# Performance work log

Hardware: AMD Instinct MI355X
Metric: run time of the kernel (lower is better)

The kernel has to match this reference:

```python
import jax, jax.numpy as jnp
import numpy as np

N_AQI, N_MEO = 35, 18
F_OUT = 16
ALPHA = 0.2


def _xavier(k, shape, gain=1.414):
    fan_in, fan_out = shape
    limit = gain * (6.0 / (fan_in + fan_out)) ** 0.5
    return jax.random.uniform(k, shape, jnp.float32, -limit, limit)


def setup_inputs() -> dict:
    key = jax.random.key(0)
    ks = jax.random.split(key, 16)
    B, T = 32, 32
    N = N_AQI + N_MEO
    out_aqi = jax.random.normal(ks[0], (B, T, N_AQI, 1), jnp.float32)
    out_meo = jax.random.normal(ks[1], (B, T, N_MEO, 3), jnp.float32)
    # sparse-ish adjacency with self loops; adj_norm is a (masked) float weight
    adj = (jax.random.uniform(ks[2], (N, N)) < 0.3).astype(jnp.float32)
    adj = adj.at[jnp.arange(N), jnp.arange(N)].set(1.0)
    adj_norm = adj * jax.random.uniform(ks[3], (N, N), jnp.float32)
    inp = {
        "out_aqi": out_aqi,
        "out_meo": out_meo,
        "adj": adj,
        "adj_norm": adj_norm,
        "W_trans": _xavier(ks[4], (1, 6), gain=1.0),
        "b_trans": jnp.zeros((6,), jnp.float32),
        "W_xa": _xavier(ks[5], (6, F_OUT)),
        "W_xm": _xavier(ks[6], (3, F_OUT)),
        "W_ua": _xavier(ks[7], (6, F_OUT)),
        "W_um": _xavier(ks[8], (3, F_OUT)),
        "a_aa": _xavier(ks[9], (2 * F_OUT + 1, 1)),
        "a_am": _xavier(ks[10], (2 * F_OUT + 1, 1)),
        "a_ma": _xavier(ks[11], (2 * F_OUT + 1, 1)),
        "a_mm": _xavier(ks[12], (2 * F_OUT + 1, 1)),
        "W_out": _xavier(ks[13], (32, 1), gain=1.0),
        "b_out": jnp.zeros((1,), jnp.float32),
    }
    return inp


def _lrelu(x):
    return jnp.where(x > 0, x, ALPHA * x)


def _edge_block(h_src, h_dst, anorm_blk, a):
    # Equivalent to matmul(cat[h_i, h_j, adj_norm_ij], a) without materializing
    # the dense (BT, Ni, Nj, 2F+1) tensor: split a into src/dst/adj parts.
    s = h_src @ a[:F_OUT, 0]                 # (BT, Ni)
    d = h_dst @ a[F_OUT:2 * F_OUT, 0]        # (BT, Nj)
    return _lrelu(s[:, :, None] + d[:, None, :] + anorm_blk[None, :, :] * a[2 * F_OUT, 0])


def reference(out_aqi, out_meo, adj, adj_norm, W_trans, b_trans, W_xa, W_xm,
              W_ua, W_um, a_aa, a_am, a_ma, a_mm, W_out, b_out):
    B, T = out_aqi.shape[:2]
    BT = B * T
    aqi = out_aqi.reshape(BT, N_AQI, 1) @ W_trans + b_trans    # (BT, 35, 6)
    meo = out_meo.reshape(BT, N_MEO, 3)                         # (BT, 18, 3)

    heter_attri = jnp.concatenate([aqi @ W_xa, meo @ W_xm], axis=1)  # (BT, 53, 16)
    h_aqi = aqi @ W_ua                                          # (BT, 35, 16)
    h_meo = meo @ W_um                                          # (BT, 18, 16)

    an = adj_norm
    e_aa = _edge_block(h_aqi, h_aqi, an[:N_AQI, :N_AQI], a_aa)
    e_am = _edge_block(h_aqi, h_meo, an[:N_AQI, N_AQI:], a_am)
    e_ma = _edge_block(h_meo, h_aqi, an[N_AQI:, :N_AQI], a_ma)
    e_mm = _edge_block(h_meo, h_meo, an[N_AQI:, N_AQI:], a_mm)
    e = jnp.concatenate([
        jnp.concatenate([e_aa, e_am], axis=2),
        jnp.concatenate([e_ma, e_mm], axis=2),
    ], axis=1)                                                  # (BT, 53, 53)

    att = jnp.where(adj[None, :, :] > 0, e, -1e12)
    att = jax.nn.softmax(att, axis=2)
    heter_out = att @ heter_attri                               # (BT, 53, 16)

    m_aqi = jnp.mean(heter_out[:, :N_AQI, :], axis=1)
    m_meo = jnp.mean(heter_out[:, N_AQI:, :], axis=1)
    out_smetric = jax.nn.sigmoid(jnp.concatenate([m_aqi, m_meo], axis=1))  # (BT, 32)
    out_sscore = jax.nn.sigmoid(out_smetric @ W_out + b_out)               # (BT, 1)
    return out_sscore, out_smetric
```

## Files before the change

kernel.cpp:

```cpp
#include <hip/hip_runtime.h>

#define N_AQI 35
#define N_MEO 18
#define NN    53
#define F     16
#define AP    20

__global__ __launch_bounds__(256)
void spat_disc_kernel(
    const float* __restrict__ out_aqi,
    const float* __restrict__ out_meo,
    const float* __restrict__ adj,
    const float* __restrict__ adj_norm,
    const float* __restrict__ W_trans,
    const float* __restrict__ b_trans,
    const float* __restrict__ W_xa,
    const float* __restrict__ W_xm,
    const float* __restrict__ W_ua,
    const float* __restrict__ W_um,
    const float* __restrict__ a_aa,
    const float* __restrict__ a_am,
    const float* __restrict__ a_ma,
    const float* __restrict__ a_mm,
    const float* __restrict__ W_out,
    const float* __restrict__ b_out,
    float* __restrict__ out, int BT)
{
  const int bt  = blockIdx.x;
  const int tid = threadIdx.x;
  const int i   = tid >> 2;
  const int fq  = tid & 3;

  __shared__ float sh_wxa[F], sh_bxa[F], sh_wua[F], sh_bua[F];
  __shared__ float sh_c[8];
  __shared__ float sh_v[12];
  __shared__ float sh_l[4];
  __shared__ float sh_dA[NN];
  __shared__ float sh_dM[NN];
  __shared__ float sh_attri[NN * AP];
  __shared__ float sh_P[NN * NN];
  __shared__ float sh_ho[NN * AP];
  __shared__ float sh_sm[32];

  if (tid < F) {
    float wxa = 0.f, bxa = 0.f, wua = 0.f, bua = 0.f;
    for (int k = 0; k < 6; ++k) {
      float wt = W_trans[k], btr = b_trans[k];
      wxa += wt  * W_xa[k * F + tid];
      bxa += btr * W_xa[k * F + tid];
      wua += wt  * W_ua[k * F + tid];
      bua += btr * W_ua[k * F + tid];
    }
    sh_wxa[tid] = wxa; sh_bxa[tid] = bxa;
    sh_wua[tid] = wua; sh_bua[tid] = bua;
  }
  __syncthreads();

  if (tid < 8) {
    const float* avec = (tid == 0 || tid == 1 || tid == 4 || tid == 5) ? a_aa
                       : (tid < 4 ? a_am : a_ma);
    int off = (tid < 4) ? 0 : F;
    const float* wv = (tid & 1) ? sh_bua : sh_wua;
    float acc = 0.f;
    for (int f = 0; f < F; ++f) acc += wv[f] * avec[off + f];
    sh_c[tid] = acc;
  } else if (tid < 20) {
    int t = tid - 8;
    int k = t % 3;
    int grp = t / 3;
    const float* avec = (grp == 0) ? a_ma : (grp == 1) ? a_mm
                       : (grp == 2) ? a_am : a_mm;
    int off = (grp < 2) ? 0 : F;
    float acc = 0.f;
    for (int f = 0; f < F; ++f) acc += W_um[k * F + f] * avec[off + f];
    sh_v[t] = acc;
  } else if (tid < 24) {
    const float* avec = (tid == 20) ? a_aa : (tid == 21) ? a_am
                       : (tid == 22) ? a_ma : a_mm;
    sh_l[tid - 20] = avec[2 * F];
  }
  __syncthreads();

  if (tid < NN) {
    if (tid < N_AQI) {
      float x = out_aqi[bt * N_AQI + tid];
      sh_dA[tid] = sh_c[4] * x + sh_c[5];
      sh_dM[tid] = sh_c[6] * x + sh_c[7];
      for (int f = 0; f < F; ++f)
        sh_attri[tid * AP + f] = sh_wxa[f] * x + sh_bxa[f];
    } else {
      int m = tid - N_AQI;
      float m0 = out_meo[(bt * N_MEO + m) * 3 + 0];
      float m1 = out_meo[(bt * N_MEO + m) * 3 + 1];
      float m2 = out_meo[(bt * N_MEO + m) * 3 + 2];
      sh_dA[tid] = m0 * sh_v[6] + m1 * sh_v[7]  + m2 * sh_v[8];
      sh_dM[tid] = m0 * sh_v[9] + m1 * sh_v[10] + m2 * sh_v[11];
      for (int f = 0; f < F; ++f)
        sh_attri[tid * AP + f] = m0 * W_xm[0 * F + f] + m1 * W_xm[1 * F + f] + m2 * W_xm[2 * F + f];
    }
  }
  for (int t = tid; t < NN * NN; t += 256) {
    int ii = t / NN;
    int jj = t - ii * NN;
    float a  = adj[t];
    float an = adj_norm[t];
    float l  = (ii < N_AQI) ? ((jj < N_AQI) ? sh_l[0] : sh_l[1])
                            : ((jj < N_AQI) ? sh_l[2] : sh_l[3]);
    sh_P[t] = (a > 0.f) ? an * l : -INFINITY;
  }
  float s0 = 0.f, s1 = 0.f;
  if (i < NN) {
    if (i < N_AQI) {
      float x = out_aqi[bt * N_AQI + i];
      s0 = sh_c[0] * x + sh_c[1];
      s1 = sh_c[2] * x + sh_c[3];
    } else {
      int m = i - N_AQI;
      float m0 = out_meo[(bt * N_MEO + m) * 3 + 0];
      float m1 = out_meo[(bt * N_MEO + m) * 3 + 1];
      float m2 = out_meo[(bt * N_MEO + m) * 3 + 2];
      s0 = m0 * sh_v[0] + m1 * sh_v[1] + m2 * sh_v[2];
      s1 = m0 * sh_v[3] + m1 * sh_v[4] + m2 * sh_v[5];
    }
  }
  __syncthreads();

  if (i < NN) {
    const float* dbase = (i < N_AQI) ? sh_dA : sh_dM;
    const float* Prow  = sh_P + i * NN;
    float a0 = 0.f, a1 = 0.f, a2 = 0.f, a3 = 0.f, lsum = 0.f;
#pragma unroll 1
    for (int j = 0; j < NN; ++j) {
      float z = ((j < N_AQI) ? s0 : s1) + dbase[j] + Prow[j];
      float e = (z > 0.0f) ? z : 0.2f * z;
      float w = __expf(e);
      lsum += w;
      const float4 av = *(const float4*)(sh_attri + j * AP + fq * 4);
      a0 += w * av.x; a1 += w * av.y; a2 += w * av.z; a3 += w * av.w;
    }
    float inv = 1.0f / lsum;
    float4* hrow = (float4*)(sh_ho + i * AP + fq * 4);
    *hrow = make_float4(a0 * inv, a1 * inv, a2 * inv, a3 * inv);
  }
  __syncthreads();

  if (tid < 32) {
    float s = 0.f;
    if (tid < F) {
      for (int r = 0; r < N_AQI; ++r) s += sh_ho[r * AP + tid];
      s *= (1.0f / N_AQI);
    } else {
      int f = tid - F;
      for (int r = N_AQI; r < NN; ++r) s += sh_ho[r * AP + f];
      s *= (1.0f / N_MEO);
    }
    float sm = 1.0f / (1.0f + __expf(-s));
    sh_sm[tid] = sm;
    out[BT + bt * 32 + tid] = sm;
  }
  __syncthreads();

  if (tid == 0) {
    float z = b_out[0];
    for (int k = 0; k < 32; ++k) z += sh_sm[k] * W_out[k];
    out[bt] = 1.0f / (1.0f + __expf(-z));
  }
}

extern "C" void kernel_launch(void* const* d_in, const int* in_sizes, int n_in,
                              void* d_out, int out_size, void* d_ws, size_t ws_size,
                              hipStream_t stream) {
  const float* out_aqi  = (const float*)d_in[0];
  const float* out_meo  = (const float*)d_in[1];
  const float* adj      = (const float*)d_in[2];
  const float* adj_norm = (const float*)d_in[3];
  const float* W_trans  = (const float*)d_in[4];
  const float* b_trans  = (const float*)d_in[5];
  const float* W_xa     = (const float*)d_in[6];
  const float* W_xm     = (const float*)d_in[7];
  const float* W_ua     = (const float*)d_in[8];
  const float* W_um     = (const float*)d_in[9];
  const float* a_aa     = (const float*)d_in[10];
  const float* a_am     = (const float*)d_in[11];
  const float* a_ma     = (const float*)d_in[12];
  const float* a_mm     = (const float*)d_in[13];
  const float* W_out    = (const float*)d_in[14];
  const float* b_out    = (const float*)d_in[15];
  float* out = (float*)d_out;

  const int BT = in_sizes[0] / N_AQI;

  spat_disc_kernel<<<BT, 256, 0, stream>>>(
      out_aqi, out_meo, adj, adj_norm, W_trans, b_trans,
      W_xa, W_xm, W_ua, W_um, a_aa, a_am, a_ma, a_mm, W_out, b_out,
      out, BT);
}
```

Baseline: 99.18 us.

## Hoist batch-invariant weight folding and masked adjacency into a precompute kernel

Adds a small precompute kernel that folds the weight products and builds the masked, scaled adjacency matrix once into workspace, instead of every one of the 1024 blocks redoing it. The main kernel now reads the P matrix straight from global memory (likely L2-cached) instead of shared memory, unrolls the inner attention loop by 4, and replaces the final serial 32-element dot product with a warp shuffle reduction. The trade-offs are an extra kernel launch and global-memory reads in the hot loop where shared-memory reads were used before, but shared memory use and per-block setup syncs go down.

```diff
diff --git a/kernel.cpp b/kernel.cpp
--- a/kernel.cpp
+++ b/kernel.cpp
@@ -5,25 +5,74 @@
 #define NN    53
 #define F     16
 #define AP    20
+#define P_OFF 64
+
+__global__ __launch_bounds__(256)
+void precompute_kernel(
+    const float* __restrict__ adj, const float* __restrict__ adj_norm,
+    const float* __restrict__ W_trans, const float* __restrict__ b_trans,
+    const float* __restrict__ W_xa, const float* __restrict__ W_ua,
+    const float* __restrict__ W_um,
+    const float* __restrict__ a_aa, const float* __restrict__ a_am,
+    const float* __restrict__ a_ma, const float* __restrict__ a_mm,
+    float* __restrict__ wsf)
+{
+  const int tid = threadIdx.x;
+  __shared__ float s_wua[F], s_bua[F];
+
+  if (blockIdx.x == 0) {
+    if (tid < F) {
+      float wxa = 0.f, bxa = 0.f, wua = 0.f, bua = 0.f;
+      for (int k = 0; k < 6; ++k) {
+        float wt = W_trans[k], btr = b_trans[k];
+        wxa += wt  * W_xa[k * F + tid];
+        bxa += btr * W_xa[k * F + tid];
+        wua += wt  * W_ua[k * F + tid];
+        bua += btr * W_ua[k * F + tid];
+      }
+      s_wua[tid] = wua; s_bua[tid] = bua;
+      wsf[20 + tid] = wxa; wsf[36 + tid] = bxa;
+    }
+    __syncthreads();
+    if (tid < 8) {
+      const float* avec = (tid == 0 || tid == 1 || tid == 4 || tid == 5) ? a_aa
+                         : (tid < 4 ? a_am : a_ma);
+      int off = (tid < 4) ? 0 : F;
+      const float* wv = (tid & 1) ? s_bua : s_wua;
+      float acc = 0.f;
+      for (int f = 0; f < F; ++f) acc += wv[f] * avec[off + f];
+      wsf[tid] = acc;
+    } else if (tid < 20) {
+      int t = tid - 8;
+      int k = t % 3;
+      int grp = t / 3;
+      const float* avec = (grp == 0) ? a_ma : (grp == 1) ? a_mm
+                         : (grp == 2) ? a_am : a_mm;
+      int off = (grp < 2) ? 0 : F;
+      float acc = 0.f;
+      for (int f = 0; f < F; ++f) acc += W_um[k * F + f] * avec[off + f];
+      wsf[8 + t] = acc;
+    }
+  }
+
+  const float l0 = a_aa[2 * F], l1 = a_am[2 * F], l2 = a_ma[2 * F], l3 = a_mm[2 * F];
+  for (int t = blockIdx.x * 256 + tid; t < NN * NN; t += 8 * 256) {
+    int ii = t / NN;
+    int jj = t - ii * NN;
+    float l = (ii < N_AQI) ? ((jj < N_AQI) ? l0 : l1)
+                           : ((jj < N_AQI) ? l2 : l3);
+    wsf[P_OFF + t] = (adj[t] > 0.f) ? adj_norm[t] * l : -INFINITY;
+  }
+}
 
 __global__ __launch_bounds__(256)
 void spat_disc_kernel(
     const float* __restrict__ out_aqi,
     const float* __restrict__ out_meo,
-    const float* __restrict__ adj,
-    const float* __restrict__ adj_norm,
-    const float* __restrict__ W_trans,
-    const float* __restrict__ b_trans,
-    const float* __restrict__ W_xa,
     const float* __restrict__ W_xm,
-    const float* __restrict__ W_ua,
-    const float* __restrict__ W_um,
-    const float* __restrict__ a_aa,
-    const float* __restrict__ a_am,
-    const float* __restrict__ a_ma,
-    const float* __restrict__ a_mm,
     const float* __restrict__ W_out,
     const float* __restrict__ b_out,
+    const float* __restrict__ wsf,
     float* __restrict__ out, int BT)
 {
   const int bt  = blockIdx.x;
@@ -31,105 +80,55 @@
   const int i   = tid >> 2;
   const int fq  = tid & 3;
 
-  __shared__ float sh_wxa[F], sh_bxa[F], sh_wua[F], sh_bua[F];
-  __shared__ float sh_c[8];
-  __shared__ float sh_v[12];
-  __shared__ float sh_l[4];
+  __shared__ float shc[52];
   __shared__ float sh_dA[NN];
   __shared__ float sh_dM[NN];
   __shared__ float sh_attri[NN * AP];
-  __shared__ float sh_P[NN * NN];
   __shared__ float sh_ho[NN * AP];
-  __shared__ float sh_sm[32];
 
-  if (tid < F) {
-    float wxa = 0.f, bxa = 0.f, wua = 0.f, bua = 0.f;
-    for (int k = 0; k < 6; ++k) {
-      float wt = W_trans[k], btr = b_trans[k];
-      wxa += wt  * W_xa[k * F + tid];
-      bxa += btr * W_xa[k * F + tid];
-      wua += wt  * W_ua[k * F + tid];
-      bua += btr * W_ua[k * F + tid];
-    }
-    sh_wxa[tid] = wxa; sh_bxa[tid] = bxa;
-    sh_wua[tid] = wua; sh_bua[tid] = bua;
-  }
-  __syncthreads();
-
-  if (tid < 8) {
-    const float* avec = (tid == 0 || tid == 1 || tid == 4 || tid == 5) ? a_aa
-                       : (tid < 4 ? a_am : a_ma);
-    int off = (tid < 4) ? 0 : F;
-    const float* wv = (tid & 1) ? sh_bua : sh_wua;
-    float acc = 0.f;
-    for (int f = 0; f < F; ++f) acc += wv[f] * avec[off + f];
-    sh_c[tid] = acc;
-  } else if (tid < 20) {
-    int t = tid - 8;
-    int k = t % 3;
-    int grp = t / 3;
-    const float* avec = (grp == 0) ? a_ma : (grp == 1) ? a_mm
-                       : (grp == 2) ? a_am : a_mm;
-    int off = (grp < 2) ? 0 : F;
-    float acc = 0.f;
-    for (int f = 0; f < F; ++f) acc += W_um[k * F + f] * avec[off + f];
-    sh_v[t] = acc;
-  } else if (tid < 24) {
-    const float* avec = (tid == 20) ? a_aa : (tid == 21) ? a_am
-                       : (tid == 22) ? a_ma : a_mm;
-    sh_l[tid - 20] = avec[2 * F];
-  }
+  if (tid < 52) shc[tid] = wsf[tid];
   __syncthreads();
 
   if (tid < NN) {
     if (tid < N_AQI) {
       float x = out_aqi[bt * N_AQI + tid];
-      sh_dA[tid] = sh_c[4] * x + sh_c[5];
-      sh_dM[tid] = sh_c[6] * x + sh_c[7];
+      sh_dA[tid] = shc[4] * x + shc[5];
+      sh_dM[tid] = shc[6] * x + shc[7];
       for (int f = 0; f < F; ++f)
-        sh_attri[tid * AP + f] = sh_wxa[f] * x + sh_bxa[f];
+        sh_attri[tid * AP + f] = shc[20 + f] * x + shc[36 + f];
     } else {
       int m = tid - N_AQI;
       float m0 = out_meo[(bt * N_MEO + m) * 3 + 0];
       float m1 = out_meo[(bt * N_MEO + m) * 3 + 1];
       float m2 = out_meo[(bt * N_MEO + m) * 3 + 2];
-      sh_dA[tid] = m0 * sh_v[6] + m1 * sh_v[7]  + m2 * sh_v[8];
-      sh_dM[tid] = m0 * sh_v[9] + m1 * sh_v[10] + m2 * sh_v[11];
+      sh_dA[tid] = m0 * shc[8 + 6] + m1 * shc[8 + 7]  + m2 * shc[8 + 8];
+      sh_dM[tid] = m0 * shc[8 + 9] + m1 * shc[8 + 10] + m2 * shc[8 + 11];
       for (int f = 0; f < F; ++f)
         sh_attri[tid * AP + f] = m0 * W_xm[0 * F + f] + m1 * W_xm[1 * F + f] + m2 * W_xm[2 * F + f];
     }
-  }
-  for (int t = tid; t < NN * NN; t += 256) {
-    int ii = t / NN;
-    int jj = t - ii * NN;
-    float a  = adj[t];
-    float an = adj_norm[t];
-    float l  = (ii < N_AQI) ? ((jj < N_AQI) ? sh_l[0] : sh_l[1])
-                            : ((jj < N_AQI) ? sh_l[2] : sh_l[3]);
-    sh_P[t] = (a > 0.f) ? an * l : -INFINITY;
   }
   float s0 = 0.f, s1 = 0.f;
   if (i < NN) {
     if (i < N_AQI) {
       float x = out_aqi[bt * N_AQI + i];
-      s0 = sh_c[0] * x + sh_c[1];
-      s1 = sh_c[2] * x + sh_c[3];
+      s0 = shc[0] * x + shc[1];
+      s1 = shc[2] * x + shc[3];
     } else {
       int m = i - N_AQI;
       float m0 = out_meo[(bt * N_MEO + m) * 3 + 0];
       float m1 = out_meo[(bt * N_MEO + m) * 3 + 1];
       float m2 = out_meo[(bt * N_MEO + m) * 3 + 2];
-      s0 = m0 * sh_v[0] + m1 * sh_v[1] + m2 * sh_v[2];
-      s1 = m0 * sh_v[3] + m1 * sh_v[4] + m2 * sh_v[5];
+      s0 = m0 * shc[8 + 0] + m1 * shc[8 + 1] + m2 * shc[8 + 2];
+      s1 = m0 * shc[8 + 3] + m1 * shc[8 + 4] + m2 * shc[8 + 5];
     }
   }
   __syncthreads();
 
   if (i < NN) {
-    const float* dbase = (i < N_AQI) ? sh_dA : sh_dM;
-    const float* Prow  = sh_P + i * NN;
+    const float* __restrict__ dbase = (i < N_AQI) ? sh_dA : sh_dM;
+    const float* __restrict__ Prow  = wsf + P_OFF + i * NN;
     float a0 = 0.f, a1 = 0.f, a2 = 0.f, a3 = 0.f, lsum = 0.f;
-#pragma unroll 1
+#pragma unroll 4
     for (int j = 0; j < NN; ++j) {
       float z = ((j < N_AQI) ? s0 : s1) + dbase[j] + Prow[j];
       float e = (z > 0.0f) ? z : 0.2f * z;
@@ -155,15 +154,12 @@
       s *= (1.0f / N_MEO);
     }
     float sm = 1.0f / (1.0f + __expf(-s));
-    sh_sm[tid] = sm;
     out[BT + bt * 32 + tid] = sm;
-  }
-  __syncthreads();
 
-  if (tid == 0) {
-    float z = b_out[0];
-    for (int k = 0; k < 32; ++k) z += sh_sm[k] * W_out[k];
-    out[bt] = 1.0f / (1.0f + __expf(-z));
+    float zc = sm * W_out[tid];
+    for (int m = 16; m > 0; m >>= 1) zc += __shfl_xor(zc, m, 32);
+    if (tid == 0)
+      out[bt] = 1.0f / (1.0f + __expf(-(zc + b_out[0])));
   }
 }
 
@@ -187,11 +183,14 @@
   const float* W_out    = (const float*)d_in[14];
   const float* b_out    = (const float*)d_in[15];
   float* out = (float*)d_out;
+  float* wsf = (float*)d_ws;
 
   const int BT = in_sizes[0] / N_AQI;
 
+  precompute_kernel<<<8, 256, 0, stream>>>(
+      adj, adj_norm, W_trans, b_trans, W_xa, W_ua, W_um,
+      a_aa, a_am, a_ma, a_mm, wsf);
+
   spat_disc_kernel<<<BT, 256, 0, stream>>>(
-      out_aqi, out_meo, adj, adj_norm, W_trans, b_trans,
-      W_xa, W_xm, W_ua, W_um, a_aa, a_am, a_ma, a_mm, W_out, b_out,
-      out, BT);
+      out_aqi, out_meo, W_xm, W_out, b_out, wsf, out, BT);
 }
```

After: 96.95 us. -2.2%, faster.
